# Performance work log

Measured on AMD Instinct MI355X. Metric: run time of the kernel, lower is better.

## Reference

```python
import jax, jax.numpy as jnp
import numpy as np

N_NODES = 16000
N_EDGES = 512000
N_TYPES = 87      # atomic numbers covered by gfn2-xtb embedding
EMBED_DIM = 28    # 16s + 8p + 4d aux basis size
NODE_DIM = 128
NUM_BASIS = 20
CUTOFF = 5.0
P_ORDER = 5       # polynomial cutoff order
MUL0, MUL1, MUL2 = 128, 64, 32  # multiplicities of 0e, 1e, 2e irreps


def setup_inputs() -> dict:
    key = jax.random.key(0)
    k1, k2, k3, k4, k5, k6 = jax.random.split(key, 6)
    at_no = jax.random.randint(k1, (N_NODES,), 1, N_TYPES)
    # spread atoms so edge distances cover (0, cutoff] and beyond
    pos = jax.random.normal(k2, (N_NODES, 3), dtype=jnp.float32) * 3.0
    src = jax.random.randint(k3, (N_EDGES,), 0, N_NODES)
    off = jax.random.randint(k4, (N_EDGES,), 1, N_NODES)  # guarantee src != dst (no zero dist)
    dst = (src + off) % N_NODES
    edge_index = jnp.stack([src, dst])
    embed_table = jax.random.normal(k5, (N_TYPES, EMBED_DIM), dtype=jnp.float32)
    W = jax.random.normal(k6, (NODE_DIM, EMBED_DIM), dtype=jnp.float32) / np.float32(np.sqrt(EMBED_DIM))
    b = jnp.zeros((NODE_DIM,), dtype=jnp.float32)  # nn.init.zeros_(bias)
    return {"at_no": at_no, "pos": pos, "edge_index": edge_index,
            "embed_table": embed_table, "W": W, "b": b}


def _sph_harm_lmax2(u):
    """e3nn real spherical harmonics l=0,1,2, normalize=True (u is unit), 'component' norm."""
    x, y, z = u[..., 0], u[..., 1], u[..., 2]
    sh0 = jnp.ones_like(x)[..., None]                       # [E,1]
    s3 = np.float32(np.sqrt(3.0))
    sh1 = s3 * u                                            # [E,3]
    s15 = np.float32(np.sqrt(15.0))
    s5 = np.float32(np.sqrt(5.0))
    sh2 = jnp.stack([
        s15 * x * z,
        s15 * x * y,
        s5 * (y * y - 0.5 * (x * x + z * z)),
        s15 * y * z,
        0.5 * s15 * (z * z - x * x),
    ], axis=-1)                                             # [E,5]
    return sh0, sh1, sh2


def reference(at_no, pos, edge_index, embed_table, W, b):
    pos = pos[:, jnp.array([1, 2, 0])]                      # axis permutation from forward()
    vec = pos[edge_index[0]] - pos[edge_index[1]]           # [E,3] edge gather
    dist = jnp.linalg.norm(vec, axis=-1, keepdims=True)     # [E,1]

    # scalar node features: Int2c1e embedding lookup + Linear
    x_scalar = embed_table[at_no] @ W.T + b                 # [N,128]

    # Bessel RBF: sqrt(2/c) * sin(n*pi*d/c) / d, n = 1..num_basis
    n = jnp.arange(1, NUM_BASIS + 1, dtype=pos.dtype)
    rbf = np.float32(np.sqrt(2.0 / CUTOFF)) * jnp.sin(n * jnp.pi * dist / CUTOFF) / dist  # [E,20]

    # polynomial cutoff (DimeNet-style, order p)
    u = dist / CUTOFF
    p = float(P_ORDER)
    ca = -(p + 1.0) * (p + 2.0) / 2.0
    cb = p * (p + 2.0)
    cc = -p * (p + 1.0) / 2.0
    fcut = jnp.where(u < 1.0,
                     1.0 + ca * u ** P_ORDER + cb * u ** (P_ORDER + 1) + cc * u ** (P_ORDER + 2),
                     0.0)                                   # [E,1]

    # real spherical harmonics on unit edge vectors, tiled per irrep multiplicity
    unit = vec / dist
    sh0, sh1, sh2 = _sph_harm_lmax2(unit)
    rsh = jnp.concatenate([jnp.tile(sh0, (1, MUL0)),
                           jnp.tile(sh1, (1, MUL1)),
                           jnp.tile(sh2, (1, MUL2))], axis=-1)  # [E, 480]

    return x_scalar, rbf, fcut, rsh
```

## Files before the change

### kernel.cpp

```cpp
#include <hip/hip_runtime.h>
#include <math.h>

#define N_NODES   16000
#define N_EDGES   512000
#define EMBED_DIM 28
#define NODE_DIM  128
#define NUM_BASIS 20

#define EPB   128
#define NBLK  (N_EDGES / EPB)

#define NODE_BLOCKS 2000
#define NODE_CHUNKS 8

#define PSTRIDE 516
#define PAT_DWORDS (8 * PSTRIDE + EPB * 4)

typedef float f32x4 __attribute__((ext_vector_type(4)));

__global__ __launch_bounds__(128) void fused_all_kernel(
    const int*   __restrict__ at_no,
    const float* __restrict__ pos,
    const int*   __restrict__ eidx,
    const float* __restrict__ embed,
    const float* __restrict__ W,
    const float* __restrict__ bias,
    float*       __restrict__ x_scalar,
    float*       __restrict__ rbf,
    float*       __restrict__ fcut,
    float*       __restrict__ rsh)
{
    const int t = threadIdx.x;

    if (blockIdx.x < NODE_BLOCKS) {
        int bid2 = blockIdx.x;
#pragma unroll 1
        for (int ch = 0; ch < NODE_CHUNKS; ++ch) {
            int idx  = (bid2 * NODE_CHUNKS + ch) * 128 + t;
            int node = idx >> 7;
            int d    = idx & 127;
            int a    = at_no[node];
            const float* er = embed + a * EMBED_DIM;
            const float* wr = W + d * EMBED_DIM;
            float sum = bias[d];
#pragma unroll
            for (int k = 0; k < EMBED_DIM; ++k)
                sum = fmaf(er[k], wr[k], sum);
            x_scalar[idx] = sum;
        }
        return;
    }

    __shared__ float sh_pat[PAT_DWORDS];
    __shared__ float sh_rbf[EPB * 20];

    const int e0 = (blockIdx.x - NODE_BLOCKS) * EPB;
    const int e  = e0 + t;

    {
        int s  = eidx[e];
        int dn = eidx[N_EDGES + e];

        float ax = pos[s*3+1],  ay = pos[s*3+2],  az = pos[s*3+0];
        float bx = pos[dn*3+1], by = pos[dn*3+2], bz = pos[dn*3+0];
        float vx = ax - bx, vy = ay - by, vz = az - bz;
        float dist = sqrtf(vx*vx + vy*vy + vz*vz);
        float inv  = 1.0f / dist;
        float ux = vx*inv, uy = vy*inv, uz = vz*inv;

        const float S3  = 1.7320508075688772f;
        const float S5  = 2.2360679774997896f;
        const float S15 = 3.8729833462074170f;
        float s0 = S3 * ux, s1 = S3 * uy, s2 = S3 * uz;
        float t0 = S15 * ux * uz;
        float t1 = S15 * ux * uy;
        float t2 = S5  * (uy*uy - 0.5f*(ux*ux + uz*uz));
        float t3 = S15 * uy * uz;
        float t4 = 0.5f * S15 * (uz*uz - ux*ux);

        f32x4* pb = (f32x4*)(sh_pat) + t;
#define PW(j, a_, b_, c_, d_) { f32x4 v_; v_.x=a_; v_.y=b_; v_.z=c_; v_.w=d_; \
                                pb[(j) * (PSTRIDE/4)] = v_; }
        PW(0, 1.0f, 1.0f, 1.0f, 1.0f)
        PW(1, s0, s1, s2, s0)
        PW(2, s1, s2, s0, s1)
        PW(3, s2, s0, s1, s2)
        PW(4, t0, t1, t2, t3)
        PW(5, t1, t2, t3, t4)
        PW(6, t2, t3, t4, t0)
        PW(7, t3, t4, t0, t1)
        PW(8, t4, t0, t1, t2)
#undef PW

        float u  = dist * 0.2f;
        float u2 = u*u, u5 = u2*u2*u;
        float f  = 1.0f + u5*(-21.0f + u*(35.0f - 15.0f*u));
        fcut[e] = (u < 1.0f) ? f : 0.0f;

        float th = 0.62831853071795864769f * dist;
        float sn = __sinf(th), cs = __cosf(th);
        float twoc = 2.0f * cs;
        float kk = 0.6324555320336759f * inv;
        float sp = 0.0f, sc = sn;
        float* rb = sh_rbf + t * 20;
#pragma unroll
        for (int q = 0; q < NUM_BASIS; ++q) {
            rb[q] = kk * sc;
            float nx = twoc*sc - sp; sp = sc; sc = nx;
        }
    }
    __syncthreads();

    {
        const f32x4* ls = (const f32x4*)sh_rbf;
        f32x4* go = (f32x4*)(rbf + (size_t)e0 * NUM_BASIS);
#pragma unroll
        for (int q = 0; q < 5; ++q)
            go[q * EPB + t] = ls[q * EPB + t];
    }

    {
        int offs[15];
#pragma unroll
        for (int k = 0; k < 15; ++k) {
            int u  = k * 128 + t;
            int d  = u / 120;
            int c  = u - d * 120;
            int p;
            if (c < 32)      p = 0;
            else if (c < 80) p = 1 + (c - 32) % 3;
            else             p = 4 + (4 * (c - 80)) % 5;
            offs[k] = p * PSTRIDE + d * 4;
        }

        float* outb = rsh + (size_t)e0 * 480 + (size_t)t * 4;
        int base = 0;

#pragma unroll 1
        for (int i = 0; i < 8; ++i) {
#pragma unroll
            for (int k = 0; k < 15; ++k) {
                f32x4 v = *(const f32x4*)(sh_pat + base + offs[k]);
                *(f32x4*)(outb + (size_t)k * 512) = v;
            }
            base += 64;
            outb += 15 * 512;
        }
    }
}

extern "C" void kernel_launch(void* const* d_in, const int* in_sizes, int n_in,
                              void* d_out, int out_size, void* d_ws, size_t ws_size,
                              hipStream_t stream) {
    const int*   at_no = (const int*)  d_in[0];
    const float* pos   = (const float*)d_in[1];
    const int*   eidx  = (const int*)  d_in[2];
    const float* embed = (const float*)d_in[3];
    const float* W     = (const float*)d_in[4];
    const float* b     = (const float*)d_in[5];

    float* out      = (float*)d_out;
    float* x_scalar = out;
    float* rbf      = x_scalar + (size_t)N_NODES * NODE_DIM;
    float* fcut     = rbf + (size_t)N_EDGES * NUM_BASIS;
    float* rsh      = fcut + N_EDGES;

    fused_all_kernel<<<NODE_BLOCKS + NBLK, 128, 0, stream>>>(
        at_no, pos, eidx, embed, W, b, x_scalar, rbf, fcut, rsh);
}
```

Baseline: 207.6 us.

## Process multiple edge chunks per block with prefetch of next chunk's positions

Each edge block now loops over four chunks of 128 edges, computing the pattern offsets once and prefetching the next chunk's edge indices and positions while the current chunk's outputs are written. The shared pattern buffer is doubled, and node work is regrouped into fewer, larger blocks. This is meant to cut per-block launch and setup overhead and hide gather latency, at the cost of fewer blocks, more shared memory per block and extra barriers.

```diff
diff --git a/kernel.cpp b/kernel.cpp
--- a/kernel.cpp
+++ b/kernel.cpp
@@ -7,11 +7,12 @@
 #define NODE_DIM  128
 #define NUM_BASIS 20
 
-#define EPB   128
-#define NBLK  (N_EDGES / EPB)
+#define EPB    128
+#define CHUNKS 4
+#define EBLK   (N_EDGES / (EPB * CHUNKS))
 
-#define NODE_BLOCKS 2000
-#define NODE_CHUNKS 8
+#define NODE_BLOCKS 500
+#define NODE_CHUNKS 32
 
 #define PSTRIDE 516
 #define PAT_DWORDS (8 * PSTRIDE + EPB * 4)
@@ -51,101 +52,118 @@
         return;
     }
 
-    __shared__ float sh_pat[PAT_DWORDS];
+    __shared__ float sh_pat[2][PAT_DWORDS];
     __shared__ float sh_rbf[EPB * 20];
 
-    const int e0 = (blockIdx.x - NODE_BLOCKS) * EPB;
-    const int e  = e0 + t;
+    const int blk = blockIdx.x - NODE_BLOCKS;
 
-    {
-        int s  = eidx[e];
-        int dn = eidx[N_EDGES + e];
+    int offs[15];
+#pragma unroll
+    for (int k = 0; k < 15; ++k) {
+        int u  = k * 128 + t;
+        int d  = u / 120;
+        int c  = u - d * 120;
+        int p;
+        if (c < 32)      p = 0;
+        else if (c < 80) p = 1 + (c - 32) % 3;
+        else             p = 4 + (4 * (c - 80)) % 5;
+        offs[k] = p * PSTRIDE + d * 4;
+    }
 
-        float ax = pos[s*3+1],  ay = pos[s*3+2],  az = pos[s*3+0];
-        float bx = pos[dn*3+1], by = pos[dn*3+2], bz = pos[dn*3+0];
-        float vx = ax - bx, vy = ay - by, vz = az - bz;
-        float dist = sqrtf(vx*vx + vy*vy + vz*vz);
-        float inv  = 1.0f / dist;
-        float ux = vx*inv, uy = vy*inv, uz = vz*inv;
+    int e = blk * (EPB * CHUNKS) + t;
+    int s  = eidx[e];
+    int dn = eidx[N_EDGES + e];
+    float ax = pos[s*3+1],  ay = pos[s*3+2],  az = pos[s*3+0];
+    float bx = pos[dn*3+1], by = pos[dn*3+2], bz = pos[dn*3+0];
 
-        const float S3  = 1.7320508075688772f;
-        const float S5  = 2.2360679774997896f;
-        const float S15 = 3.8729833462074170f;
-        float s0 = S3 * ux, s1 = S3 * uy, s2 = S3 * uz;
-        float t0 = S15 * ux * uz;
-        float t1 = S15 * ux * uy;
-        float t2 = S5  * (uy*uy - 0.5f*(ux*ux + uz*uz));
-        float t3 = S15 * uy * uz;
-        float t4 = 0.5f * S15 * (uz*uz - ux*ux);
+#pragma unroll 1
+    for (int c = 0; c < CHUNKS; ++c) {
+        const int ecur = blk * (EPB * CHUNKS) + c * EPB + t;
+        const int ebase = blk * (EPB * CHUNKS) + c * EPB;
 
-        f32x4* pb = (f32x4*)(sh_pat) + t;
+        {
+            float vx = ax - bx, vy = ay - by, vz = az - bz;
+            float dist = sqrtf(vx*vx + vy*vy + vz*vz);
+            float inv  = 1.0f / dist;
+            float ux = vx*inv, uy = vy*inv, uz = vz*inv;
+
+            const float S3  = 1.7320508075688772f;
+            const float S5  = 2.2360679774997896f;
+            const float S15 = 3.8729833462074170f;
+            float s0 = S3 * ux, s1 = S3 * uy, s2 = S3 * uz;
+            float t0 = S15 * ux * uz;
+            float t1 = S15 * ux * uy;
+            float t2 = S5  * (uy*uy - 0.5f*(ux*ux + uz*uz));
+            float t3 = S15 * uy * uz;
+            float t4 = 0.5f * S15 * (uz*uz - ux*ux);
+
+            f32x4* pb = (f32x4*)(&sh_pat[c & 1][0]) + t;
 #define PW(j, a_, b_, c_, d_) { f32x4 v_; v_.x=a_; v_.y=b_; v_.z=c_; v_.w=d_; \
                                 pb[(j) * (PSTRIDE/4)] = v_; }
-        PW(0, 1.0f, 1.0f, 1.0f, 1.0f)
-        PW(1, s0, s1, s2, s0)
-        PW(2, s1, s2, s0, s1)
-        PW(3, s2, s0, s1, s2)
-        PW(4, t0, t1, t2, t3)
-        PW(5, t1, t2, t3, t4)
-        PW(6, t2, t3, t4, t0)
-        PW(7, t3, t4, t0, t1)
-        PW(8, t4, t0, t1, t2)
+            PW(0, 1.0f, 1.0f, 1.0f, 1.0f)
+            PW(1, s0, s1, s2, s0)
+            PW(2, s1, s2, s0, s1)
+            PW(3, s2, s0, s1, s2)
+            PW(4, t0, t1, t2, t3)
+            PW(5, t1, t2, t3, t4)
+            PW(6, t2, t3, t4, t0)
+            PW(7, t3, t4, t0, t1)
+            PW(8, t4, t0, t1, t2)
 #undef PW
 
-        float u  = dist * 0.2f;
-        float u2 = u*u, u5 = u2*u2*u;
-        float f  = 1.0f + u5*(-21.0f + u*(35.0f - 15.0f*u));
-        fcut[e] = (u < 1.0f) ? f : 0.0f;
+            float u  = dist * 0.2f;
+            float u2 = u*u, u5 = u2*u2*u;
+            float f  = 1.0f + u5*(-21.0f + u*(35.0f - 15.0f*u));
+            fcut[ecur] = (u < 1.0f) ? f : 0.0f;
 
-        float th = 0.62831853071795864769f * dist;
-        float sn = __sinf(th), cs = __cosf(th);
-        float twoc = 2.0f * cs;
-        float kk = 0.6324555320336759f * inv;
-        float sp = 0.0f, sc = sn;
-        float* rb = sh_rbf + t * 20;
+            float th = 0.62831853071795864769f * dist;
+            float sn = __sinf(th), cs = __cosf(th);
+            float twoc = 2.0f * cs;
+            float kk = 0.6324555320336759f * inv;
+            float sp = 0.0f, sc = sn;
+            float* rb = sh_rbf + t * 20;
 #pragma unroll
-        for (int q = 0; q < NUM_BASIS; ++q) {
-            rb[q] = kk * sc;
-            float nx = twoc*sc - sp; sp = sc; sc = nx;
-        }
-    }
-    __syncthreads();
-
-    {
-        const f32x4* ls = (const f32x4*)sh_rbf;
-        f32x4* go = (f32x4*)(rbf + (size_t)e0 * NUM_BASIS);
-#pragma unroll
-        for (int q = 0; q < 5; ++q)
-            go[q * EPB + t] = ls[q * EPB + t];
-    }
-
-    {
-        int offs[15];
-#pragma unroll
-        for (int k = 0; k < 15; ++k) {
-            int u  = k * 128 + t;
-            int d  = u / 120;
-            int c  = u - d * 120;
-            int p;
-            if (c < 32)      p = 0;
-            else if (c < 80) p = 1 + (c - 32) % 3;
-            else             p = 4 + (4 * (c - 80)) % 5;
-            offs[k] = p * PSTRIDE + d * 4;
+            for (int q = 0; q < NUM_BASIS; ++q) {
+                rb[q] = kk * sc;
+                float nx = twoc*sc - sp; sp = sc; sc = nx;
+            }
         }
 
-        float* outb = rsh + (size_t)e0 * 480 + (size_t)t * 4;
-        int base = 0;
+        if (c + 1 < CHUNKS) {
+            int en = ecur + EPB;
+            s  = eidx[en];
+            dn = eidx[N_EDGES + en];
+            ax = pos[s*3+1];  ay = pos[s*3+2];  az = pos[s*3+0];
+            bx = pos[dn*3+1]; by = pos[dn*3+2]; bz = pos[dn*3+0];
+        }
 
+        __syncthreads();
+
+        {
+            const f32x4* ls = (const f32x4*)sh_rbf;
+            f32x4* go = (f32x4*)(rbf + (size_t)ebase * NUM_BASIS);
+#pragma unroll
+            for (int q = 0; q < 5; ++q)
+                go[q * EPB + t] = ls[q * EPB + t];
+        }
+
+        {
+            const float* patb = &sh_pat[c & 1][0];
+            float* outb = rsh + (size_t)ebase * 480 + (size_t)t * 4;
+            int base = 0;
 #pragma unroll 1
-        for (int i = 0; i < 8; ++i) {
+            for (int i = 0; i < 8; ++i) {
 #pragma unroll
-            for (int k = 0; k < 15; ++k) {
-                f32x4 v = *(const f32x4*)(sh_pat + base + offs[k]);
-                *(f32x4*)(outb + (size_t)k * 512) = v;
+                for (int k = 0; k < 15; ++k) {
+                    f32x4 v = *(const f32x4*)(patb + base + offs[k]);
+                    *(f32x4*)(outb + (size_t)k * 512) = v;
+                }
+                base += 64;
+                outb += 15 * 512;
             }
-            base += 64;
-            outb += 15 * 512;
         }
+
+        __syncthreads();
     }
 }
 
@@ -165,6 +183,6 @@
     float* fcut     = rbf + (size_t)N_EDGES * NUM_BASIS;
     float* rsh      = fcut + N_EDGES;
 
-    fused_all_kernel<<<NODE_BLOCKS + NBLK, 128, 0, stream>>>(
+    fused_all_kernel<<<NODE_BLOCKS + EBLK, 128, 0, stream>>>(
         at_no, pos, eidx, embed, W, b, x_scalar, rbf, fcut, rsh);
 }
```

New measurement: 204.2 us. About the same (-1.7%).

## Convert fused kernel to persistent single-wave blocks with atomic work queue

Applied to the files above, without the earlier changes.

Replaces the one-block-per-tile launch with a fixed grid of 64-thread blocks. Each block pulls edge tiles or node-linear chunks from an atomic counter that is zeroed by a memset before launch. Edge tiles shrink to 64 edges, so each block is a single wavefront and the block barrier can go. The aim is to cut launch and tail scheduling overhead and balance node and edge work. The cost is an extra memset operation, atomic contention on one counter, and smaller tiles in a kernel that is mostly store-bandwidth bound.

```diff
diff --git a/kernel.cpp b/kernel.cpp
--- a/kernel.cpp
+++ b/kernel.cpp
@@ -7,18 +7,20 @@
 #define NODE_DIM  128
 #define NUM_BASIS 20
 
-#define EPB   128
-#define NBLK  (N_EDGES / EPB)
+#define EPB             64
+#define EDGE_ITEMS      (N_EDGES / EPB)
+#define NODE_ITEM_ELEMS 2048
+#define NODE_ITEMS      ((N_NODES * NODE_DIM) / NODE_ITEM_ELEMS)
+#define TOTAL_ITEMS     (EDGE_ITEMS + NODE_ITEMS)
 
-#define NODE_BLOCKS 2000
-#define NODE_CHUNKS 8
+#define PSTRIDE    260
+#define PAT_DWORDS (8 * PSTRIDE + EPB * 4)
 
-#define PSTRIDE 516
-#define PAT_DWORDS (8 * PSTRIDE + EPB * 4)
+#define GRID_BLOCKS 2816
 
 typedef float f32x4 __attribute__((ext_vector_type(4)));
 
-__global__ __launch_bounds__(128) void fused_all_kernel(
+__global__ __launch_bounds__(64) void persist_kernel(
     const int*   __restrict__ at_no,
     const float* __restrict__ pos,
     const int*   __restrict__ eidx,
@@ -28,123 +30,135 @@
     float*       __restrict__ x_scalar,
     float*       __restrict__ rbf,
     float*       __restrict__ fcut,
-    float*       __restrict__ rsh)
+    float*       __restrict__ rsh,
+    unsigned*                 ctr)
 {
     const int t = threadIdx.x;
 
-    if (blockIdx.x < NODE_BLOCKS) {
-        int bid2 = blockIdx.x;
-#pragma unroll 1
-        for (int ch = 0; ch < NODE_CHUNKS; ++ch) {
-            int idx  = (bid2 * NODE_CHUNKS + ch) * 128 + t;
-            int node = idx >> 7;
-            int d    = idx & 127;
-            int a    = at_no[node];
-            const float* er = embed + a * EMBED_DIM;
-            const float* wr = W + d * EMBED_DIM;
-            float sum = bias[d];
+    __shared__ float sh_pat[PAT_DWORDS];
+    __shared__ float sh_rbf[EPB * NUM_BASIS];
+
+    int offs[15];
 #pragma unroll
-            for (int k = 0; k < EMBED_DIM; ++k)
-                sum = fmaf(er[k], wr[k], sum);
-            x_scalar[idx] = sum;
-        }
-        return;
+    for (int k = 0; k < 15; ++k) {
+        int u = k * 64 + t;
+        int d = u / 120;
+        int c = u - d * 120;
+        int p;
+        if (c < 32)      p = 0;
+        else if (c < 80) p = 1 + (c - 32) % 3;
+        else             p = 4 + (4 * (c - 80)) % 5;
+        offs[k] = p * PSTRIDE + d * 4;
     }
 
-    __shared__ float sh_pat[PAT_DWORDS];
-    __shared__ float sh_rbf[EPB * 20];
+    int it_static = blockIdx.x;
 
-    const int e0 = (blockIdx.x - NODE_BLOCKS) * EPB;
-    const int e  = e0 + t;
+    for (;;) {
+        int item;
+        if (ctr) {
+            if (t == 0) item = (int)atomicAdd(ctr, 1u);
+            item = __shfl(item, 0);
+        } else {
+            item = it_static;
+            it_static += GRID_BLOCKS;
+        }
+        if (item >= TOTAL_ITEMS) return;
 
-    {
-        int s  = eidx[e];
-        int dn = eidx[N_EDGES + e];
+        if (item < EDGE_ITEMS) {
+            const int e0 = item * EPB;
+            const int e  = e0 + t;
 
-        float ax = pos[s*3+1],  ay = pos[s*3+2],  az = pos[s*3+0];
-        float bx = pos[dn*3+1], by = pos[dn*3+2], bz = pos[dn*3+0];
-        float vx = ax - bx, vy = ay - by, vz = az - bz;
-        float dist = sqrtf(vx*vx + vy*vy + vz*vz);
-        float inv  = 1.0f / dist;
-        float ux = vx*inv, uy = vy*inv, uz = vz*inv;
+            {
+                int s  = eidx[e];
+                int dn = eidx[N_EDGES + e];
 
-        const float S3  = 1.7320508075688772f;
-        const float S5  = 2.2360679774997896f;
-        const float S15 = 3.8729833462074170f;
-        float s0 = S3 * ux, s1 = S3 * uy, s2 = S3 * uz;
-        float t0 = S15 * ux * uz;
-        float t1 = S15 * ux * uy;
-        float t2 = S5  * (uy*uy - 0.5f*(ux*ux + uz*uz));
-        float t3 = S15 * uy * uz;
-        float t4 = 0.5f * S15 * (uz*uz - ux*ux);
+                float ax = pos[s*3+1],  ay = pos[s*3+2],  az = pos[s*3+0];
+                float bx = pos[dn*3+1], by = pos[dn*3+2], bz = pos[dn*3+0];
+                float vx = ax - bx, vy = ay - by, vz = az - bz;
+                float dist = sqrtf(vx*vx + vy*vy + vz*vz);
+                float inv  = 1.0f / dist;
+                float ux = vx*inv, uy = vy*inv, uz = vz*inv;
 
-        f32x4* pb = (f32x4*)(sh_pat) + t;
+                const float S3  = 1.7320508075688772f;
+                const float S5  = 2.2360679774997896f;
+                const float S15 = 3.8729833462074170f;
+                float s0 = S3 * ux, s1 = S3 * uy, s2 = S3 * uz;
+                float t0 = S15 * ux * uz;
+                float t1 = S15 * ux * uy;
+                float t2 = S5  * (uy*uy - 0.5f*(ux*ux + uz*uz));
+                float t3 = S15 * uy * uz;
+                float t4 = 0.5f * S15 * (uz*uz - ux*ux);
+
+                f32x4* pb = (f32x4*)sh_pat + t;
 #define PW(j, a_, b_, c_, d_) { f32x4 v_; v_.x=a_; v_.y=b_; v_.z=c_; v_.w=d_; \
                                 pb[(j) * (PSTRIDE/4)] = v_; }
-        PW(0, 1.0f, 1.0f, 1.0f, 1.0f)
-        PW(1, s0, s1, s2, s0)
-        PW(2, s1, s2, s0, s1)
-        PW(3, s2, s0, s1, s2)
-        PW(4, t0, t1, t2, t3)
-        PW(5, t1, t2, t3, t4)
-        PW(6, t2, t3, t4, t0)
-        PW(7, t3, t4, t0, t1)
-        PW(8, t4, t0, t1, t2)
+                PW(0, 1.0f, 1.0f, 1.0f, 1.0f)
+                PW(1, s0, s1, s2, s0)
+                PW(2, s1, s2, s0, s1)
+                PW(3, s2, s0, s1, s2)
+                PW(4, t0, t1, t2, t3)
+                PW(5, t1, t2, t3, t4)
+                PW(6, t2, t3, t4, t0)
+                PW(7, t3, t4, t0, t1)
+                PW(8, t4, t0, t1, t2)
 #undef PW
 
-        float u  = dist * 0.2f;
-        float u2 = u*u, u5 = u2*u2*u;
-        float f  = 1.0f + u5*(-21.0f + u*(35.0f - 15.0f*u));
-        fcut[e] = (u < 1.0f) ? f : 0.0f;
+                float u  = dist * 0.2f;
+                float u2 = u*u, u5 = u2*u2*u;
+                float f  = 1.0f + u5*(-21.0f + u*(35.0f - 15.0f*u));
+                fcut[e] = (u < 1.0f) ? f : 0.0f;
 
-        float th = 0.62831853071795864769f * dist;
-        float sn = __sinf(th), cs = __cosf(th);
-        float twoc = 2.0f * cs;
-        float kk = 0.6324555320336759f * inv;
-        float sp = 0.0f, sc = sn;
-        float* rb = sh_rbf + t * 20;
+                float th = 0.62831853071795864769f * dist;
+                float sn = __sinf(th), cs = __cosf(th);
+                float twoc = 2.0f * cs;
+                float kk = 0.6324555320336759f * inv;
+                float sp = 0.0f, sc = sn;
+                float* rb = sh_rbf + t * NUM_BASIS;
 #pragma unroll
-        for (int q = 0; q < NUM_BASIS; ++q) {
-            rb[q] = kk * sc;
-            float nx = twoc*sc - sp; sp = sc; sc = nx;
-        }
-    }
-    __syncthreads();
+                for (int q = 0; q < NUM_BASIS; ++q) {
+                    rb[q] = kk * sc;
+                    float nx = twoc*sc - sp; sp = sc; sc = nx;
+                }
+            }
 
-    {
-        const f32x4* ls = (const f32x4*)sh_rbf;
-        f32x4* go = (f32x4*)(rbf + (size_t)e0 * NUM_BASIS);
+            {
+                const f32x4* ls = (const f32x4*)sh_rbf;
+                f32x4* go = (f32x4*)(rbf + (size_t)e0 * NUM_BASIS);
 #pragma unroll
-        for (int q = 0; q < 5; ++q)
-            go[q * EPB + t] = ls[q * EPB + t];
-    }
+                for (int q = 0; q < 5; ++q)
+                    go[q * 64 + t] = ls[q * 64 + t];
+            }
 
-    {
-        int offs[15];
+            {
+                float* outb = rsh + (size_t)e0 * 480 + (size_t)t * 4;
+                int base = 0;
+#pragma unroll 1
+                for (int o = 0; o < 8; ++o) {
 #pragma unroll
-        for (int k = 0; k < 15; ++k) {
-            int u  = k * 128 + t;
-            int d  = u / 120;
-            int c  = u - d * 120;
-            int p;
-            if (c < 32)      p = 0;
-            else if (c < 80) p = 1 + (c - 32) % 3;
-            else             p = 4 + (4 * (c - 80)) % 5;
-            offs[k] = p * PSTRIDE + d * 4;
-        }
-
-        float* outb = rsh + (size_t)e0 * 480 + (size_t)t * 4;
-        int base = 0;
-
+                    for (int k = 0; k < 15; ++k) {
+                        f32x4 v = *(const f32x4*)(sh_pat + base + offs[k]);
+                        *(f32x4*)(outb + (size_t)k * 256) = v;
+                    }
+                    base += 32;
+                    outb += 15 * 256;
+                }
+            }
+        } else {
+            const int nb = (item - EDGE_ITEMS) * NODE_ITEM_ELEMS;
 #pragma unroll 1
-        for (int i = 0; i < 8; ++i) {
+            for (int j = 0; j < NODE_ITEM_ELEMS / 64; ++j) {
+                int idx  = nb + j * 64 + t;
+                int node = idx >> 7;
+                int d    = idx & 127;
+                int a    = at_no[node];
+                const float* er = embed + a * EMBED_DIM;
+                const float* wr = W + d * EMBED_DIM;
+                float sum = bias[d];
 #pragma unroll
-            for (int k = 0; k < 15; ++k) {
-                f32x4 v = *(const f32x4*)(sh_pat + base + offs[k]);
-                *(f32x4*)(outb + (size_t)k * 512) = v;
+                for (int k = 0; k < EMBED_DIM; ++k)
+                    sum = fmaf(er[k], wr[k], sum);
+                x_scalar[idx] = sum;
             }
-            base += 64;
-            outb += 15 * 512;
         }
     }
 }
@@ -165,6 +179,12 @@
     float* fcut     = rbf + (size_t)N_EDGES * NUM_BASIS;
     float* rsh      = fcut + N_EDGES;
 
-    fused_all_kernel<<<NODE_BLOCKS + NBLK, 128, 0, stream>>>(
-        at_no, pos, eidx, embed, W, b, x_scalar, rbf, fcut, rsh);
+    unsigned* ctr = nullptr;
+    if (ws_size >= 4) {
+        ctr = (unsigned*)d_ws;
+        hipMemsetAsync(ctr, 0, 4, stream);
+    }
+
+    persist_kernel<<<GRID_BLOCKS, 64, 0, stream>>>(
+        at_no, pos, eidx, embed, W, b, x_scalar, rbf, fcut, rsh, ctr);
 }
```

Result: slower. 239.3 us (+15.3%).
